# Optimization experiments

Measured on AMD Instinct MI355X. Metric: run time of the kernel, lower is better.

Reference implementation:

```python
import jax, jax.numpy as jnp
import numpy as np

T, HID, H, KV, D = 2048, 2048, 16, 8, 128
EPS = 1e-6
THETA = 10000.0


def setup_inputs() -> dict:
    key = jax.random.key(0)
    ks = jax.random.split(key, 6)
    positions = jnp.arange(T, dtype=jnp.int64 if jax.config.jax_enable_x64 else jnp.int32)
    hidden_states = jax.random.normal(ks[0], (T, HID), dtype=jnp.float32)
    scale = 0.02
    Wq = jax.random.normal(ks[1], (HID, H * 2 * D), dtype=jnp.float32) * scale
    Wk = jax.random.normal(ks[2], (HID, KV * D), dtype=jnp.float32) * scale
    Wv = jax.random.normal(ks[3], (HID, KV * D), dtype=jnp.float32) * scale
    Wo = jax.random.normal(ks[4], (H * D, HID), dtype=jnp.float32) * scale
    q_norm_w = jnp.zeros((D,), dtype=jnp.float32)  # torch init: zeros, applied as (1+w)
    k_norm_w = jnp.zeros((D,), dtype=jnp.float32)
    return {"positions": positions, "hidden_states": hidden_states, "Wq": Wq,
            "Wk": Wk, "Wv": Wv, "Wo": Wo, "q_norm_w": q_norm_w, "k_norm_w": k_norm_w}


def _rms_norm(x, w):
    # fp32 RMSNorm with (1 + weight) scaling, per last dim
    xf = x.astype(jnp.float32)
    inv = jax.lax.rsqrt(jnp.mean(xf * xf, axis=-1, keepdims=True) + EPS)
    return (xf * inv * (1.0 + w.astype(jnp.float32))).astype(x.dtype)


def _rope(x, positions):
    # neox-style rotary over full head_dim; x: (T, heads, D)
    half = D // 2
    inv_freq = 1.0 / (THETA ** (jnp.arange(0, half, dtype=jnp.float32) / half))
    freqs = positions.astype(jnp.float32)[:, None] * inv_freq  # (T, half)
    cos = jnp.cos(freqs)[:, None, :]  # (T,1,half)
    sin = jnp.sin(freqs)[:, None, :]
    x1, x2 = x[..., :half], x[..., half:]
    return jnp.concatenate([x1 * cos - x2 * sin, x2 * cos + x1 * sin], axis=-1)


def reference(positions, hidden_states, Wq, Wk, Wv, Wo, q_norm_w, k_norm_w):
    scaling = D ** -0.5
    qg = (hidden_states @ Wq).reshape(T, H, 2 * D)
    q, gate = qg[..., :D], qg[..., D:]              # (T,H,D) each
    k = (hidden_states @ Wk).reshape(T, KV, D)
    v = (hidden_states @ Wv).reshape(T, KV, D)
    q = _rms_norm(q, q_norm_w)
    k = _rms_norm(k, k_norm_w)
    q = _rope(q, positions)
    k = _rope(k, positions)
    # GQA: repeat kv heads
    rep = H // KV
    k = jnp.repeat(k, rep, axis=1)                   # (T,H,D)
    v = jnp.repeat(v, rep, axis=1)
    scores = jnp.einsum('thd,shd->hts', q, k) * scaling  # (H,T,T)
    causal = positions[:, None] >= positions[None, :]     # (T,T)
    scores = jnp.where(causal[None], scores, jnp.finfo(scores.dtype).min)
    probs = jax.nn.softmax(scores, axis=-1)
    o = jnp.einsum('hts,shd->thd', probs, v).reshape(T, H * D)
    o = o * jax.nn.sigmoid(gate.reshape(T, H * D))
    return o @ Wo
```

## Files before the change

### kernel.cpp

```cpp
#include <hip/hip_runtime.h>
#include <stdint.h>
#include <math.h>

#define T_SEQ 2048
#define HID   2048
#define NH    16
#define NKV   8
#define DH    128

typedef __bf16 bf16x8 __attribute__((ext_vector_type(8)));
typedef float  f32x4  __attribute__((ext_vector_type(4)));

__device__ __forceinline__ ushort f2bf(float f) {
  uint32_t u = __float_as_uint(f);
  u += 0x7FFF + ((u >> 16) & 1);
  return (ushort)(u >> 16);
}
__device__ __forceinline__ ushort f2bf_rz(float f) {
  return (ushort)(__float_as_uint(f) >> 16);
}
__device__ __forceinline__ float bf2f(ushort u) {
  return __uint_as_float(((uint32_t)u) << 16);
}
__device__ __forceinline__ void gld16(const void* g, void* l) {
  __builtin_amdgcn_global_load_lds(
      (const __attribute__((address_space(1))) uint32_t*)g,
      (__attribute__((address_space(3))) uint32_t*)l, 16, 0, 0);
}

__global__ __launch_bounds__(256) void prep_kernel(
    const float* __restrict__ hs, const float* __restrict__ Wq,
    const float* __restrict__ Wk, const float* __restrict__ Wv,
    const float* __restrict__ Wo, ushort* __restrict__ hs16,
    ushort* __restrict__ Wqt, ushort* __restrict__ Wkt,
    ushort* __restrict__ Wvt, ushort* __restrict__ Wot) {
  __shared__ float tile[32][33];
  int bid = blockIdx.x;
  if (bid < 4096) {
    int i = (bid * 256 + threadIdx.x) * 4;
    float4 v = *(const float4*)(hs + i);
    ushort4 o = {f2bf(v.x), f2bf(v.y), f2bf(v.z), f2bf(v.w)};
    *(ushort4*)(hs16 + i) = o;
    return;
  }
  bid -= 4096;
  const float* src; ushort* dst; int N, bi, bj;
  if (bid < 8192)       { src = Wq; dst = Wqt; N = 4096; bj = bid & 127; bi = bid >> 7; }
  else if (bid < 10240) { bid -= 8192;  src = Wk; dst = Wkt; N = 1024; bj = bid & 31; bi = bid >> 5; }
  else if (bid < 12288) { bid -= 10240; src = Wv; dst = Wvt; N = 1024; bj = bid & 31; bi = bid >> 5; }
  else                  { bid -= 12288; src = Wo; dst = Wot; N = 2048; bj = bid & 63; bi = bid >> 6; }
  int row = threadIdx.x >> 3, c4 = (threadIdx.x & 7) * 4;
  float4 v = *(const float4*)(src + (size_t)(bi * 32 + row) * N + bj * 32 + c4);
  tile[row][c4 + 0] = v.x; tile[row][c4 + 1] = v.y;
  tile[row][c4 + 2] = v.z; tile[row][c4 + 3] = v.w;
  __syncthreads();
  ushort4 o = {f2bf(tile[c4 + 0][row]), f2bf(tile[c4 + 1][row]),
               f2bf(tile[c4 + 2][row]), f2bf(tile[c4 + 3][row])};
  *(ushort4*)(dst + (size_t)(bj * 32 + row) * HID + bi * 32 + c4) = o;
}

template <int MI>
__device__ __forceinline__ void gemm_loop(
    const ushort* __restrict__ A, const ushort* __restrict__ Bt,
    int K, int m0, int n0, ushort* As, ushort* Bs, f32x4 (*acc)[4]) {
  const int tid = threadIdx.x, lane = tid & 63, w = tid >> 6;
  const int quad = lane >> 4, l15 = lane & 15;
  const int wm = (w >> 1) * (MI * 16), wn = (w & 1) * 64;
  const int srow = tid >> 2, sch = tid & 3;
  for (int k0 = 0; k0 < K; k0 += 32) {
    __syncthreads();
#pragma unroll
    for (int p = 0; p < MI / 2; ++p) {
      int row = p * 64 + srow;
      int gch = sch ^ ((row >> 1) & 3);
      gld16(A + (size_t)(m0 + row) * K + k0 + gch * 8,
            As + (p * 256 + w * 64) * 8);
    }
#pragma unroll
    for (int p = 0; p < 2; ++p) {
      int row = p * 64 + srow;
      int gch = sch ^ ((row >> 1) & 3);
      gld16(Bt + (size_t)(n0 + row) * K + k0 + gch * 8,
            Bs + (p * 256 + w * 64) * 8);
    }
    __syncthreads();
    bf16x8 af[MI], bfr[4];
#pragma unroll
    for (int mi = 0; mi < MI; ++mi) {
      int row = wm + mi * 16 + l15;
      int pch = quad ^ ((row >> 1) & 3);
      af[mi] = *(const bf16x8*)(As + row * 32 + pch * 8);
    }
#pragma unroll
    for (int ni = 0; ni < 4; ++ni) {
      int row = wn + ni * 16 + l15;
      int pch = quad ^ ((row >> 1) & 3);
      bfr[ni] = *(const bf16x8*)(Bs + row * 32 + pch * 8);
    }
#pragma unroll
    for (int mi = 0; mi < MI; ++mi)
#pragma unroll
      for (int ni = 0; ni < 4; ++ni)
        acc[mi][ni] = __builtin_amdgcn_mfma_f32_16x16x32_bf16(
            af[mi], bfr[ni], acc[mi][ni], 0, 0, 0);
  }
}

__device__ __forceinline__ void bf16_store(f32x4 (*acc)[4],
                                           ushort* __restrict__ Cb, int Ncols,
                                           int m0, int n0) {
  const int lane = threadIdx.x & 63, w = threadIdx.x >> 6;
  const int quad = lane >> 4, l15 = lane & 15;
  const int wm = (w >> 1) * 64, wn = (w & 1) * 64;
#pragma unroll
  for (int mi = 0; mi < 4; ++mi)
#pragma unroll
    for (int ni = 0; ni < 4; ++ni)
#pragma unroll
      for (int r = 0; r < 4; ++r) {
        int row = m0 + wm + mi * 16 + quad * 4 + r;
        int col = n0 + wn + ni * 16 + l15;
        Cb[(size_t)row * Ncols + col] = f2bf(acc[mi][ni][r]);
      }
}

__device__ __forceinline__ void norm_rope_epilogue(
    f32x4 (*acc)[4], const float* __restrict__ wgt,
    const int* __restrict__ positions, int m0, ushort* __restrict__ outp,
    int ostride, char* smem) {
  ushort* tile = (ushort*)smem;
  float* ssum = (float*)(smem + 34816);
  const int tid = threadIdx.x, lane = tid & 63, w = tid >> 6;
  const int quad = lane >> 4, l15 = lane & 15;
  const int wm = (w >> 1) * 64, wn = (w & 1) * 64;
  float sp[4][4];
#pragma unroll
  for (int mi = 0; mi < 4; ++mi)
#pragma unroll
    for (int r = 0; r < 4; ++r) {
      float s = 0.f;
#pragma unroll
      for (int ni = 0; ni < 4; ++ni) { float v = acc[mi][ni][r]; s += v * v; }
#pragma unroll
      for (int off = 1; off <= 8; off <<= 1) s += __shfl_xor(s, off, 64);
      sp[mi][r] = s;
    }
  if (l15 == 0) {
#pragma unroll
    for (int mi = 0; mi < 4; ++mi)
#pragma unroll
      for (int r = 0; r < 4; ++r)
        ssum[(w & 1) * 128 + wm + mi * 16 + quad * 4 + r] = sp[mi][r];
  }
  __syncthreads();
  float wv[4];
#pragma unroll
  for (int ni = 0; ni < 4; ++ni) wv[ni] = 1.f + wgt[wn + ni * 16 + l15];
#pragma unroll
  for (int mi = 0; mi < 4; ++mi)
#pragma unroll
    for (int r = 0; r < 4; ++r) {
      int row = wm + mi * 16 + quad * 4 + r;
      float inv = rsqrtf((ssum[row] + ssum[128 + row]) * (1.f / 128.f) + 1e-6f);
#pragma unroll
      for (int ni = 0; ni < 4; ++ni)
        tile[row * 136 + wn + ni * 16 + l15] =
            f2bf(acc[mi][ni][r] * inv * wv[ni]);
    }
  __syncthreads();
  const int row = tid >> 1, d0 = (tid & 1) * 32;
  const float pos = (float)positions[m0 + row];
  __align__(16) ushort lo[32], hi[32];
#pragma unroll
  for (int j = 0; j < 32; ++j) {
    int d = d0 + j;
    float rev = pos * exp2f((float)d * -0.20762050593045233f) *
                0.15915494309189535f;
    float fr = rev - floorf(rev);
    float s = __builtin_amdgcn_sinf(fr);
    float c = __builtin_amdgcn_cosf(fr);
    float x1 = bf2f(tile[row * 136 + d]);
    float x2 = bf2f(tile[row * 136 + d + 64]);
    lo[j] = f2bf(x1 * c - x2 * s);
    hi[j] = f2bf(x2 * c + x1 * s);
  }
  ushort* op = outp + (size_t)(m0 + row) * ostride + d0;
#pragma unroll
  for (int j = 0; j < 4; ++j) {
    *((uint4*)op + j)        = ((const uint4*)lo)[j];
    *((uint4*)(op + 64) + j) = ((const uint4*)hi)[j];
  }
}

__global__ __launch_bounds__(256) void gemm_qkv(
    const ushort* __restrict__ hs16, const ushort* __restrict__ Wqt,
    const ushort* __restrict__ Wkt, const ushort* __restrict__ Wvt,
    const int* __restrict__ positions, const float* __restrict__ qnw,
    const float* __restrict__ knw, ushort* __restrict__ q16,
    ushort* __restrict__ gate16, ushort* __restrict__ k16,
    ushort* __restrict__ v16t) {
  __shared__ __align__(16) char smem[35840 + 1024];
  ushort* As = (ushort*)smem;
  ushort* Bs = As + 4096;
  f32x4 acc[4][4];
#pragma unroll
  for (int i = 0; i < 4; ++i)
#pragma unroll
    for (int j = 0; j < 4; ++j) acc[i][j] = (f32x4){0.f, 0.f, 0.f, 0.f};
  const int b = blockIdx.x;
  if (b < 512) {
    int mt = b >> 5, nt = b & 31, m0 = mt * 128, h = nt >> 1;
    gemm_loop<4>(hs16, Wqt, HID, m0, nt * 128, As, Bs, acc);
    if ((nt & 1) == 0)
      norm_rope_epilogue(acc, qnw, positions, m0, q16 + h * DH, NH * DH, smem);
    else
      bf16_store(acc, gate16, NH * DH, m0, h * DH);
  } else if (b < 640) {
    int f = b - 512, mt = f >> 3, nt = f & 7, m0 = mt * 128;
    gemm_loop<4>(hs16, Wkt, HID, m0, nt * 128, As, Bs, acc);
    norm_rope_epilogue(acc, knw, positions, m0, k16 + nt * DH, NKV * DH, smem);
  } else {
    int f = b - 640, mt = f >> 4, nt = f & 15;
    gemm_loop<4>(Wvt, hs16, HID, mt * 128, nt * 128, As, Bs, acc);
    bf16_store(acc, v16t, T_SEQ, mt * 128, nt * 128);
  }
}

__global__ __launch_bounds__(256) void gemm_out(
    const ushort* __restrict__ ob16, const ushort* __restrict__ Wot,
    float* __restrict__ out) {
  __shared__ ushort As[64 * 32];
  __shared__ ushort Bs[128 * 32];
  f32x4 acc[2][4];
#pragma unroll
  for (int i = 0; i < 2; ++i)
#pragma unroll
    for (int j = 0; j < 4; ++j) acc[i][j] = (f32x4){0.f, 0.f, 0.f, 0.f};
  const int b = blockIdx.x;
  const int m0 = (b >> 4) * 64, n0 = (b & 15) * 128;
  gemm_loop<2>(ob16, Wot, HID, m0, n0, As, Bs, acc);
  const int lane = threadIdx.x & 63, w = threadIdx.x >> 6;
  const int quad = lane >> 4, l15 = lane & 15;
  const int wm = (w >> 1) * 32, wn = (w & 1) * 64;
#pragma unroll
  for (int mi = 0; mi < 2; ++mi)
#pragma unroll
    for (int ni = 0; ni < 4; ++ni)
#pragma unroll
      for (int r = 0; r < 4; ++r) {
        int row = m0 + wm + mi * 16 + quad * 4 + r;
        int col = n0 + wn + ni * 16 + l15;
        out[(size_t)row * HID + col] = acc[mi][ni][r];
      }
}

__global__ __launch_bounds__(256) void attn_mfma(
    const ushort* __restrict__ q16, const ushort* __restrict__ k16,
    const ushort* __restrict__ v16t, const float* __restrict__ qnw,
    const float* __restrict__ knw, ushort* __restrict__ Op0,
    ushort* __restrict__ Op1, float* __restrict__ lpart) {
  const int pb = blockIdx.x, h = blockIdx.y, s = blockIdx.z, kvh = h >> 1;
  const int tid = threadIdx.x, lane = tid & 63, w = tid >> 6;
  const int quad = lane >> 4, l15 = lane & 15;

  __shared__ ushort Ks[2][64 * 128];
  __shared__ ushort Vs[2][144 * 64];
  __shared__ ushort Ps[4][16][72];

#pragma unroll
  for (int buf = 0; buf < 2; ++buf)
    for (int i = tid; i < 16 * 64; i += 256) {
      int row = 128 + (i >> 6), col = i & 63;
      Vs[buf][row * 64 + col] = (row == 128) ? (ushort)0x3F80 : (ushort)0;
    }

  __shared__ float s8[8];
  __shared__ float bshare;
  {
    float mq = 0.f, mk = 0.f;
    if (tid < 128) { mq = fabsf(1.f + qnw[tid]); mk = fabsf(1.f + knw[tid]); }
#pragma unroll
    for (int off = 32; off >= 1; off >>= 1) {
      mq = fmaxf(mq, __shfl_xor(mq, off, 64));
      mk = fmaxf(mk, __shfl_xor(mk, off, 64));
    }
    if (lane == 0) { s8[w * 2] = mq; s8[w * 2 + 1] = mk; }
    __syncthreads();
    if (tid == 0) {
      float MQ = fmaxf(s8[0], s8[2]), MK = fmaxf(s8[1], s8[3]);
      bshare = 16.3217f * MQ * MK * 1.02f + 0.1f;
    }
    __syncthreads();
  }
  const float B = bshare;
  const float CSC = 0.08838834764831845f * 1.44269504088896f;

#pragma unroll 1
  for (int sel = 0; sel < 2; ++sel) {
    const int qt = sel ? (31 - pb) : pb;
    const int q0 = qt * 64, nk = qt + 1;
    const int ntl = (nk > s) ? ((nk - s + 1) >> 1) : 0;

    bf16x8 qf[4];
    const ushort* qbase = q16 + ((size_t)(q0 + w * 16 + l15) * NH + h) * DH;
#pragma unroll
    for (int ks = 0; ks < 4; ++ks)
      qf[ks] = *(const bf16x8*)(qbase + ks * 32 + quad * 8);

    f32x4 oacc[9];
#pragma unroll
    for (int i = 0; i < 9; ++i) oacc[i] = (f32x4){0.f, 0.f, 0.f, 0.f};

    __syncthreads();
    if (ntl > 0) {
      const int kt0 = s * 64;
#pragma unroll
      for (int p = 0; p < 4; ++p) {
        int row = p * 16 + (tid >> 4), ch = tid & 15;
        int gch = ch ^ (row & 15);
        gld16(k16 + ((size_t)(kt0 + row) * NKV + kvh) * DH + gch * 8,
              (ushort*)Ks[0] + (p * 256 + w * 64) * 8);
      }
#pragma unroll
      for (int p = 0; p < 4; ++p) {
        int row = p * 32 + (tid >> 3), ch = tid & 7;
        int gch = ch ^ (row & 7);
        gld16(v16t + (size_t)(kvh * DH + row) * T_SEQ + kt0 + gch * 8,
              (ushort*)Vs[0] + (p * 256 + w * 64) * 8);
      }
    }

#pragma unroll 1
    for (int it = 0; it < ntl; ++it) {
      const int kt = s + 2 * it;
      const int cur = it & 1;
      __syncthreads();
      if (it + 1 < ntl) {
        const int nt0 = (kt + 2) * 64;
#pragma unroll
        for (int p = 0; p < 4; ++p) {
          int row = p * 16 + (tid >> 4), ch = tid & 15;
          int gch = ch ^ (row & 15);
          gld16(k16 + ((size_t)(nt0 + row) * NKV + kvh) * DH + gch * 8,
                (ushort*)Ks[1 - cur] + (p * 256 + w * 64) * 8);
        }
#pragma unroll
        for (int p = 0; p < 4; ++p) {
          int row = p * 32 + (tid >> 3), ch = tid & 7;
          int gch = ch ^ (row & 7);
          gld16(v16t + (size_t)(kvh * DH + row) * T_SEQ + nt0 + gch * 8,
                (ushort*)Vs[1 - cur] + (p * 256 + w * 64) * 8);
        }
      }

      f32x4 sacc[4];
#pragma unroll
      for (int ni = 0; ni < 4; ++ni) sacc[ni] = (f32x4){0.f, 0.f, 0.f, 0.f};
      const ushort* KsC = Ks[cur];
#pragma unroll
      for (int ks = 0; ks < 4; ++ks)
#pragma unroll
        for (int ni = 0; ni < 4; ++ni) {
          int row = ni * 16 + l15;
          int pch = (ks * 4 + quad) ^ (row & 15);
          bf16x8 kf = *(const bf16x8*)(KsC + row * 128 + pch * 8);
          sacc[ni] = __builtin_amdgcn_mfma_f32_16x16x32_bf16(
              qf[ks], kf, sacc[ni], 0, 0, 0);
        }

      const bool diag = (kt == qt);
      const int kt0 = kt * 64;
#pragma unroll
      for (int ni = 0; ni < 4; ++ni) {
        int key = kt0 + ni * 16 + l15;
#pragma unroll
        for (int r = 0; r < 4; ++r) {
          float arg = fmaf(sacc[ni][r], CSC, -B);
          float pv;
          if (diag) {
            int q = q0 + w * 16 + quad * 4 + r;
            pv = (key <= q) ? exp2f(arg) : 0.f;
          } else {
            pv = exp2f(arg);
          }
          Ps[w][quad * 4 + r][ni * 16 + l15] = f2bf_rz(pv);
        }
      }

      const ushort* VsC = Vs[cur];
#pragma unroll
      for (int ks2 = 0; ks2 < 2; ++ks2) {
        bf16x8 pf = *(const bf16x8*)(&Ps[w][l15][ks2 * 32 + quad * 8]);
#pragma unroll
        for (int ni = 0; ni < 9; ++ni) {
          int row = ni * 16 + l15;
          int pch = (ks2 * 4 + quad) ^ (row & 7);
          bf16x8 vf = *(const bf16x8*)(VsC + row * 64 + pch * 8);
          oacc[ni] = __builtin_amdgcn_mfma_f32_16x16x32_bf16(
              pf, vf, oacc[ni], 0, 0, 0);
        }
      }
    }

    ushort* Op = s ? Op1 : Op0;
#pragma unroll
    for (int ni = 0; ni < 8; ++ni) {
      int d = ni * 16 + l15;
#pragma unroll
      for (int r = 0; r < 4; ++r) {
        int q = q0 + w * 16 + quad * 4 + r;
        Op[((size_t)h * T_SEQ + q) * DH + d] = f2bf(oacc[ni][r]);
      }
    }
    if (l15 == 0) {
#pragma unroll
      for (int r = 0; r < 4; ++r) {
        int q = q0 + w * 16 + quad * 4 + r;
        lpart[(size_t)s * (NH * T_SEQ) + h * T_SEQ + q] = oacc[8][r];
      }
    }
  }
}

__global__ __launch_bounds__(256) void combine_kernel(
    const ushort* __restrict__ Op0, const ushort* __restrict__ Op1,
    const float* __restrict__ lpart, const ushort* __restrict__ gate16,
    ushort* __restrict__ ob16) {
  const int t = blockIdx.x, tid = threadIdx.x;
  const int h = tid >> 4, d0 = (tid & 15) * 8;
  const float l = lpart[h * T_SEQ + t] + lpart[NH * T_SEQ + h * T_SEQ + t];
  const float inv = 1.0f / l;
  const size_t po = ((size_t)h * T_SEQ + t) * DH + d0;
  ushort4 a0 = *(const ushort4*)(Op0 + po);
  ushort4 a1 = *(const ushort4*)(Op0 + po + 4);
  ushort4 b0 = *(const ushort4*)(Op1 + po);
  ushort4 b1 = *(const ushort4*)(Op1 + po + 4);
  const ushort* gp = gate16 + (size_t)t * (NH * DH) + h * DH + d0;
  ushort4 g0 = *(const ushort4*)(gp);
  ushort4 g1 = *(const ushort4*)(gp + 4);
  float oa[8] = {bf2f(a0.x), bf2f(a0.y), bf2f(a0.z), bf2f(a0.w),
                 bf2f(a1.x), bf2f(a1.y), bf2f(a1.z), bf2f(a1.w)};
  float ob[8] = {bf2f(b0.x), bf2f(b0.y), bf2f(b0.z), bf2f(b0.w),
                 bf2f(b1.x), bf2f(b1.y), bf2f(b1.z), bf2f(b1.w)};
  float gg[8] = {bf2f(g0.x), bf2f(g0.y), bf2f(g0.z), bf2f(g0.w),
                 bf2f(g1.x), bf2f(g1.y), bf2f(g1.z), bf2f(g1.w)};
  ushort r[8];
#pragma unroll
  for (int i = 0; i < 8; ++i) {
    float o = (oa[i] + ob[i]) * inv;
    o = o / (1.0f + exp2f(-gg[i] * 1.44269504088896f));
    r[i] = f2bf(o);
  }
  ushort* op = ob16 + (size_t)t * (NH * DH) + h * DH + d0;
  *(ushort4*)(op)     = (ushort4){r[0], r[1], r[2], r[3]};
  *(ushort4*)(op + 4) = (ushort4){r[4], r[5], r[6], r[7]};
}

extern "C" void kernel_launch(void* const* d_in, const int* in_sizes, int n_in,
                              void* d_out, int out_size, void* d_ws, size_t ws_size,
                              hipStream_t stream) {
  const int*   positions = (const int*)d_in[0];
  const float* hs  = (const float*)d_in[1];
  const float* Wq  = (const float*)d_in[2];
  const float* Wk  = (const float*)d_in[3];
  const float* Wv  = (const float*)d_in[4];
  const float* Wo  = (const float*)d_in[5];
  const float* qnw = (const float*)d_in[6];
  const float* knw = (const float*)d_in[7];
  float* out = (float*)d_out;

  const size_t MB = 1 << 20;
  uint8_t* ws = (uint8_t*)d_ws;
  ushort* hs16  = (ushort*)(ws + 0);
  ushort* Op0   = (ushort*)(ws + 0);
  ushort* Wqt   = (ushort*)(ws + 8 * MB);
  ushort* Op1   = (ushort*)(ws + 8 * MB);
  ushort* ob16  = (ushort*)(ws + 16 * MB);
  ushort* Wkt   = (ushort*)(ws + 24 * MB);
  float*  lpart = (float*)(ws + 24 * MB);
  ushort* Wvt   = (ushort*)(ws + 28 * MB);
  ushort* gate16= (ushort*)(ws + 32 * MB);
  ushort* q16   = (ushort*)(ws + 40 * MB);
  ushort* k16   = (ushort*)(ws + 48 * MB);
  ushort* v16t  = (ushort*)(ws + 52 * MB);
  ushort* Wot   = (ushort*)(ws + 56 * MB);

  prep_kernel<<<20480, 256, 0, stream>>>(hs, Wq, Wk, Wv, Wo,
                                         hs16, Wqt, Wkt, Wvt, Wot);
  gemm_qkv<<<768, 256, 0, stream>>>(hs16, Wqt, Wkt, Wvt, positions, qnw, knw,
                                    q16, gate16, k16, v16t);
  attn_mfma<<<dim3(16, NH, 2), 256, 0, stream>>>(q16, k16, v16t, qnw, knw,
                                                 Op0, Op1, lpart);
  combine_kernel<<<T_SEQ, 256, 0, stream>>>(Op0, Op1, lpart, gate16, ob16);
  gemm_out<<<512, 256, 0, stream>>>(ob16, Wot, out);
}
```

Before: 297.5 us.

## Split attention KV across three slices, move q norm/rope into attention, add norm_k kernel

Several changes land together. The weight transpose in prep uses 64x64 tiles with wider stores. The QKV GEMM now writes raw bf16 outputs, and a separate norm_k kernel applies RMSNorm and rope to K. Q norm and rope are folded into the attention kernel's Q load. The KV split goes from 2 to 3 slices with single buffering, which drops the K/V prefetch double-buffer, and combine now sums three partials. The goal is more attention parallelism and a lighter GEMM epilogue, at the cost of an extra launch, lost load/compute overlap, and more partial-output traffic.

```diff
diff --git a/kernel.cpp b/kernel.cpp
--- a/kernel.cpp
+++ b/kernel.cpp
@@ -34,7 +34,6 @@
     const float* __restrict__ Wo, ushort* __restrict__ hs16,
     ushort* __restrict__ Wqt, ushort* __restrict__ Wkt,
     ushort* __restrict__ Wvt, ushort* __restrict__ Wot) {
-  __shared__ float tile[32][33];
   int bid = blockIdx.x;
   if (bid < 4096) {
     int i = (bid * 256 + threadIdx.x) * 4;
@@ -45,18 +44,28 @@
   }
   bid -= 4096;
   const float* src; ushort* dst; int N, bi, bj;
-  if (bid < 8192)       { src = Wq; dst = Wqt; N = 4096; bj = bid & 127; bi = bid >> 7; }
-  else if (bid < 10240) { bid -= 8192;  src = Wk; dst = Wkt; N = 1024; bj = bid & 31; bi = bid >> 5; }
-  else if (bid < 12288) { bid -= 10240; src = Wv; dst = Wvt; N = 1024; bj = bid & 31; bi = bid >> 5; }
-  else                  { bid -= 12288; src = Wo; dst = Wot; N = 2048; bj = bid & 63; bi = bid >> 6; }
-  int row = threadIdx.x >> 3, c4 = (threadIdx.x & 7) * 4;
-  float4 v = *(const float4*)(src + (size_t)(bi * 32 + row) * N + bj * 32 + c4);
-  tile[row][c4 + 0] = v.x; tile[row][c4 + 1] = v.y;
-  tile[row][c4 + 2] = v.z; tile[row][c4 + 3] = v.w;
+  if (bid < 2048)      { src = Wq; dst = Wqt; N = 4096; bj = bid & 63; bi = bid >> 6; }
+  else if (bid < 2560) { bid -= 2048; src = Wk; dst = Wkt; N = 1024; bj = bid & 15; bi = bid >> 4; }
+  else if (bid < 3072) { bid -= 2560; src = Wv; dst = Wvt; N = 1024; bj = bid & 15; bi = bid >> 4; }
+  else                 { bid -= 3072; src = Wo; dst = Wot; N = 2048; bj = bid & 31; bi = bid >> 5; }
+  __shared__ float tile[64][65];
+  const int r = threadIdx.x >> 2, cg = (threadIdx.x & 3) * 16;
+  const float* sp = src + (size_t)(bi * 64 + r) * N + bj * 64 + cg;
+#pragma unroll
+  for (int p = 0; p < 4; ++p) {
+    float4 v = *(const float4*)(sp + p * 4);
+    tile[r][cg + p * 4 + 0] = v.x; tile[r][cg + p * 4 + 1] = v.y;
+    tile[r][cg + p * 4 + 2] = v.z; tile[r][cg + p * 4 + 3] = v.w;
+  }
   __syncthreads();
-  ushort4 o = {f2bf(tile[c4 + 0][row]), f2bf(tile[c4 + 1][row]),
-               f2bf(tile[c4 + 2][row]), f2bf(tile[c4 + 3][row])};
-  *(ushort4*)(dst + (size_t)(bj * 32 + row) * HID + bi * 32 + c4) = o;
+  ushort* dp = dst + (size_t)(bj * 64 + r) * HID + bi * 64 + cg;
+#pragma unroll
+  for (int p = 0; p < 2; ++p) {
+    union { uint4 v; ushort u[8]; } o;
+#pragma unroll
+    for (int j = 0; j < 8; ++j) o.u[j] = f2bf(tile[cg + p * 8 + j][r]);
+    *(uint4*)(dp + p * 8) = o.v;
+  }
 }
 
 template <int MI>
@@ -124,84 +133,13 @@
       }
 }
 
-__device__ __forceinline__ void norm_rope_epilogue(
-    f32x4 (*acc)[4], const float* __restrict__ wgt,
-    const int* __restrict__ positions, int m0, ushort* __restrict__ outp,
-    int ostride, char* smem) {
-  ushort* tile = (ushort*)smem;
-  float* ssum = (float*)(smem + 34816);
-  const int tid = threadIdx.x, lane = tid & 63, w = tid >> 6;
-  const int quad = lane >> 4, l15 = lane & 15;
-  const int wm = (w >> 1) * 64, wn = (w & 1) * 64;
-  float sp[4][4];
-#pragma unroll
-  for (int mi = 0; mi < 4; ++mi)
-#pragma unroll
-    for (int r = 0; r < 4; ++r) {
-      float s = 0.f;
-#pragma unroll
-      for (int ni = 0; ni < 4; ++ni) { float v = acc[mi][ni][r]; s += v * v; }
-#pragma unroll
-      for (int off = 1; off <= 8; off <<= 1) s += __shfl_xor(s, off, 64);
-      sp[mi][r] = s;
-    }
-  if (l15 == 0) {
-#pragma unroll
-    for (int mi = 0; mi < 4; ++mi)
-#pragma unroll
-      for (int r = 0; r < 4; ++r)
-        ssum[(w & 1) * 128 + wm + mi * 16 + quad * 4 + r] = sp[mi][r];
-  }
-  __syncthreads();
-  float wv[4];
-#pragma unroll
-  for (int ni = 0; ni < 4; ++ni) wv[ni] = 1.f + wgt[wn + ni * 16 + l15];
-#pragma unroll
-  for (int mi = 0; mi < 4; ++mi)
-#pragma unroll
-    for (int r = 0; r < 4; ++r) {
-      int row = wm + mi * 16 + quad * 4 + r;
-      float inv = rsqrtf((ssum[row] + ssum[128 + row]) * (1.f / 128.f) + 1e-6f);
-#pragma unroll
-      for (int ni = 0; ni < 4; ++ni)
-        tile[row * 136 + wn + ni * 16 + l15] =
-            f2bf(acc[mi][ni][r] * inv * wv[ni]);
-    }
-  __syncthreads();
-  const int row = tid >> 1, d0 = (tid & 1) * 32;
-  const float pos = (float)positions[m0 + row];
-  __align__(16) ushort lo[32], hi[32];
-#pragma unroll
-  for (int j = 0; j < 32; ++j) {
-    int d = d0 + j;
-    float rev = pos * exp2f((float)d * -0.20762050593045233f) *
-                0.15915494309189535f;
-    float fr = rev - floorf(rev);
-    float s = __builtin_amdgcn_sinf(fr);
-    float c = __builtin_amdgcn_cosf(fr);
-    float x1 = bf2f(tile[row * 136 + d]);
-    float x2 = bf2f(tile[row * 136 + d + 64]);
-    lo[j] = f2bf(x1 * c - x2 * s);
-    hi[j] = f2bf(x2 * c + x1 * s);
-  }
-  ushort* op = outp + (size_t)(m0 + row) * ostride + d0;
-#pragma unroll
-  for (int j = 0; j < 4; ++j) {
-    *((uint4*)op + j)        = ((const uint4*)lo)[j];
-    *((uint4*)(op + 64) + j) = ((const uint4*)hi)[j];
-  }
-}
-
 __global__ __launch_bounds__(256) void gemm_qkv(
     const ushort* __restrict__ hs16, const ushort* __restrict__ Wqt,
     const ushort* __restrict__ Wkt, const ushort* __restrict__ Wvt,
-    const int* __restrict__ positions, const float* __restrict__ qnw,
-    const float* __restrict__ knw, ushort* __restrict__ q16,
-    ushort* __restrict__ gate16, ushort* __restrict__ k16,
+    ushort* __restrict__ qg16, ushort* __restrict__ kb16,
     ushort* __restrict__ v16t) {
-  __shared__ __align__(16) char smem[35840 + 1024];
-  ushort* As = (ushort*)smem;
-  ushort* Bs = As + 4096;
+  __shared__ ushort As[128 * 32];
+  __shared__ ushort Bs[128 * 32];
   f32x4 acc[4][4];
 #pragma unroll
   for (int i = 0; i < 4; ++i)
@@ -209,20 +147,17 @@
     for (int j = 0; j < 4; ++j) acc[i][j] = (f32x4){0.f, 0.f, 0.f, 0.f};
   const int b = blockIdx.x;
   if (b < 512) {
-    int mt = b >> 5, nt = b & 31, m0 = mt * 128, h = nt >> 1;
-    gemm_loop<4>(hs16, Wqt, HID, m0, nt * 128, As, Bs, acc);
-    if ((nt & 1) == 0)
-      norm_rope_epilogue(acc, qnw, positions, m0, q16 + h * DH, NH * DH, smem);
-    else
-      bf16_store(acc, gate16, NH * DH, m0, h * DH);
+    int m0 = (b >> 5) * 128, n0 = (b & 31) * 128;
+    gemm_loop<4>(hs16, Wqt, HID, m0, n0, As, Bs, acc);
+    bf16_store(acc, qg16, 4096, m0, n0);
   } else if (b < 640) {
-    int f = b - 512, mt = f >> 3, nt = f & 7, m0 = mt * 128;
-    gemm_loop<4>(hs16, Wkt, HID, m0, nt * 128, As, Bs, acc);
-    norm_rope_epilogue(acc, knw, positions, m0, k16 + nt * DH, NKV * DH, smem);
+    int f = b - 512, m0 = (f >> 3) * 128, n0 = (f & 7) * 128;
+    gemm_loop<4>(hs16, Wkt, HID, m0, n0, As, Bs, acc);
+    bf16_store(acc, kb16, 1024, m0, n0);
   } else {
-    int f = b - 640, mt = f >> 4, nt = f & 15;
-    gemm_loop<4>(Wvt, hs16, HID, mt * 128, nt * 128, As, Bs, acc);
-    bf16_store(acc, v16t, T_SEQ, mt * 128, nt * 128);
+    int f = b - 640, m0 = (f >> 4) * 128, n0 = (f & 15) * 128;
+    gemm_loop<4>(Wvt, hs16, HID, m0, n0, As, Bs, acc);
+    bf16_store(acc, v16t, T_SEQ, m0, n0);
   }
 }
 
@@ -254,25 +189,55 @@
       }
 }
 
+__global__ __launch_bounds__(128) void norm_k(
+    const ushort* __restrict__ kb16, const int* __restrict__ positions,
+    const float* __restrict__ kw, ushort* __restrict__ k16) {
+  const int t = blockIdx.x, kv = blockIdx.y, d = threadIdx.x;
+  const ushort* x = kb16 + ((size_t)t * NKV + kv) * DH;
+  ushort* out = k16 + ((size_t)t * NKV + kv) * DH;
+  float v = bf2f(x[d]);
+  float ss = v * v;
+#pragma unroll
+  for (int off = 32; off >= 1; off >>= 1) ss += __shfl_xor(ss, off, 64);
+  __shared__ float red[2];
+  if ((d & 63) == 0) red[d >> 6] = ss;
+  __syncthreads();
+  float mean = (red[0] + red[1]) * (1.0f / 128.0f);
+  float xn = v * rsqrtf(mean + 1e-6f) * (1.0f + kw[d]);
+  __shared__ float sh[128];
+  sh[d] = xn;
+  __syncthreads();
+  if (d < 64) {
+    float pos = (float)positions[t];
+    float rev = pos * exp2f((float)d * -0.20762050593045233f) *
+                0.15915494309189535f;
+    float fr = rev - floorf(rev);
+    float s = __builtin_amdgcn_sinf(fr);
+    float c = __builtin_amdgcn_cosf(fr);
+    float x1 = sh[d], x2 = sh[d + 64];
+    out[d]      = f2bf(x1 * c - x2 * s);
+    out[d + 64] = f2bf(x2 * c + x1 * s);
+  }
+}
+
 __global__ __launch_bounds__(256) void attn_mfma(
-    const ushort* __restrict__ q16, const ushort* __restrict__ k16,
-    const ushort* __restrict__ v16t, const float* __restrict__ qnw,
-    const float* __restrict__ knw, ushort* __restrict__ Op0,
-    ushort* __restrict__ Op1, float* __restrict__ lpart) {
+    const ushort* __restrict__ qg16, const ushort* __restrict__ k16,
+    const ushort* __restrict__ v16t, const int* __restrict__ positions,
+    const float* __restrict__ qnw, const float* __restrict__ knw,
+    ushort* __restrict__ Op0, ushort* __restrict__ Op1,
+    ushort* __restrict__ Op2, float* __restrict__ lpart) {
   const int pb = blockIdx.x, h = blockIdx.y, s = blockIdx.z, kvh = h >> 1;
   const int tid = threadIdx.x, lane = tid & 63, w = tid >> 6;
   const int quad = lane >> 4, l15 = lane & 15;
 
-  __shared__ ushort Ks[2][64 * 128];
-  __shared__ ushort Vs[2][144 * 64];
+  __shared__ ushort Ks[64 * 128];
+  __shared__ ushort Vs[144 * 64];
   __shared__ ushort Ps[4][16][72];
 
-#pragma unroll
-  for (int buf = 0; buf < 2; ++buf)
-    for (int i = tid; i < 16 * 64; i += 256) {
-      int row = 128 + (i >> 6), col = i & 63;
-      Vs[buf][row * 64 + col] = (row == 128) ? (ushort)0x3F80 : (ushort)0;
-    }
+  for (int i = tid; i < 16 * 64; i += 256) {
+    int row = 128 + (i >> 6), col = i & 63;
+    Vs[row * 64 + col] = (row == 128) ? (ushort)0x3F80 : (ushort)0;
+  }
 
   __shared__ float s8[8];
   __shared__ float bshare;
@@ -295,81 +260,95 @@
   const float B = bshare;
   const float CSC = 0.08838834764831845f * 1.44269504088896f;
 
+  float wq[4][8];
+#pragma unroll
+  for (int ks = 0; ks < 4; ++ks)
+#pragma unroll
+    for (int j = 0; j < 8; ++j) wq[ks][j] = 1.f + qnw[ks * 32 + quad * 8 + j];
+
 #pragma unroll 1
   for (int sel = 0; sel < 2; ++sel) {
     const int qt = sel ? (31 - pb) : pb;
-    const int q0 = qt * 64, nk = qt + 1;
-    const int ntl = (nk > s) ? ((nk - s + 1) >> 1) : 0;
-
-    bf16x8 qf[4];
-    const ushort* qbase = q16 + ((size_t)(q0 + w * 16 + l15) * NH + h) * DH;
+    const int q0 = qt * 64;
+    const int ntl = (qt >= s) ? ((qt - s) / 3 + 1) : 0;
+
+    float qv[4][8];
+    const ushort* qb = qg16 + ((size_t)(q0 + w * 16 + l15) * NH + h) * (2 * DH);
+#pragma unroll
+    for (int ks = 0; ks < 4; ++ks) {
+      ushort4 u0 = *(const ushort4*)(qb + ks * 32 + quad * 8);
+      ushort4 u1 = *(const ushort4*)(qb + ks * 32 + quad * 8 + 4);
+      qv[ks][0] = bf2f(u0.x); qv[ks][1] = bf2f(u0.y);
+      qv[ks][2] = bf2f(u0.z); qv[ks][3] = bf2f(u0.w);
+      qv[ks][4] = bf2f(u1.x); qv[ks][5] = bf2f(u1.y);
+      qv[ks][6] = bf2f(u1.z); qv[ks][7] = bf2f(u1.w);
+    }
+    float ss = 0.f;
 #pragma unroll
     for (int ks = 0; ks < 4; ++ks)
-      qf[ks] = *(const bf16x8*)(qbase + ks * 32 + quad * 8);
+#pragma unroll
+      for (int j = 0; j < 8; ++j) ss += qv[ks][j] * qv[ks][j];
+    ss += __shfl_xor(ss, 16, 64);
+    ss += __shfl_xor(ss, 32, 64);
+    const float inv = rsqrtf(ss * (1.f / 128.f) + 1e-6f);
+    const float pos = (float)positions[q0 + w * 16 + l15];
+    union { bf16x8 v; ushort u[8]; } qfu[4];
+#pragma unroll
+    for (int ks = 0; ks < 2; ++ks)
+#pragma unroll
+      for (int j = 0; j < 8; ++j) {
+        int d = ks * 32 + quad * 8 + j;
+        float rev = pos * exp2f((float)d * -0.20762050593045233f) *
+                    0.15915494309189535f;
+        float fr = rev - floorf(rev);
+        float sn = __builtin_amdgcn_sinf(fr);
+        float cs = __builtin_amdgcn_cosf(fr);
+        float x1 = qv[ks][j] * inv * wq[ks][j];
+        float x2 = qv[ks + 2][j] * inv * wq[ks + 2][j];
+        qfu[ks].u[j]     = f2bf(x1 * cs - x2 * sn);
+        qfu[ks + 2].u[j] = f2bf(x2 * cs + x1 * sn);
+      }
 
     f32x4 oacc[9];
 #pragma unroll
     for (int i = 0; i < 9; ++i) oacc[i] = (f32x4){0.f, 0.f, 0.f, 0.f};
 
-    __syncthreads();
-    if (ntl > 0) {
-      const int kt0 = s * 64;
+#pragma unroll 1
+    for (int it = 0; it < ntl; ++it) {
+      const int kt = s + 3 * it;
+      const int kt0 = kt * 64;
+      __syncthreads();
 #pragma unroll
       for (int p = 0; p < 4; ++p) {
         int row = p * 16 + (tid >> 4), ch = tid & 15;
         int gch = ch ^ (row & 15);
         gld16(k16 + ((size_t)(kt0 + row) * NKV + kvh) * DH + gch * 8,
-              (ushort*)Ks[0] + (p * 256 + w * 64) * 8);
+              Ks + (p * 256 + w * 64) * 8);
       }
 #pragma unroll
       for (int p = 0; p < 4; ++p) {
         int row = p * 32 + (tid >> 3), ch = tid & 7;
         int gch = ch ^ (row & 7);
         gld16(v16t + (size_t)(kvh * DH + row) * T_SEQ + kt0 + gch * 8,
-              (ushort*)Vs[0] + (p * 256 + w * 64) * 8);
-      }
-    }
-
-#pragma unroll 1
-    for (int it = 0; it < ntl; ++it) {
-      const int kt = s + 2 * it;
-      const int cur = it & 1;
+              Vs + (p * 256 + w * 64) * 8);
+      }
       __syncthreads();
-      if (it + 1 < ntl) {
-        const int nt0 = (kt + 2) * 64;
-#pragma unroll
-        for (int p = 0; p < 4; ++p) {
-          int row = p * 16 + (tid >> 4), ch = tid & 15;
-          int gch = ch ^ (row & 15);
-          gld16(k16 + ((size_t)(nt0 + row) * NKV + kvh) * DH + gch * 8,
-                (ushort*)Ks[1 - cur] + (p * 256 + w * 64) * 8);
-        }
-#pragma unroll
-        for (int p = 0; p < 4; ++p) {
-          int row = p * 32 + (tid >> 3), ch = tid & 7;
-          int gch = ch ^ (row & 7);
-          gld16(v16t + (size_t)(kvh * DH + row) * T_SEQ + nt0 + gch * 8,
-                (ushort*)Vs[1 - cur] + (p * 256 + w * 64) * 8);
-        }
-      }
 
       f32x4 sacc[4];
 #pragma unroll
       for (int ni = 0; ni < 4; ++ni) sacc[ni] = (f32x4){0.f, 0.f, 0.f, 0.f};
-      const ushort* KsC = Ks[cur];
 #pragma unroll
       for (int ks = 0; ks < 4; ++ks)
 #pragma unroll
         for (int ni = 0; ni < 4; ++ni) {
           int row = ni * 16 + l15;
           int pch = (ks * 4 + quad) ^ (row & 15);
-          bf16x8 kf = *(const bf16x8*)(KsC + row * 128 + pch * 8);
+          bf16x8 kf = *(const bf16x8*)(Ks + row * 128 + pch * 8);
           sacc[ni] = __builtin_amdgcn_mfma_f32_16x16x32_bf16(
-              qf[ks], kf, sacc[ni], 0, 0, 0);
+              qfu[ks].v, kf, sacc[ni], 0, 0, 0);
         }
 
       const bool diag = (kt == qt);
-      const int kt0 = kt * 64;
 #pragma unroll
       for (int ni = 0; ni < 4; ++ni) {
         int key = kt0 + ni * 16 + l15;
@@ -387,7 +366,6 @@
         }
       }
 
-      const ushort* VsC = Vs[cur];
 #pragma unroll
       for (int ks2 = 0; ks2 < 2; ++ks2) {
         bf16x8 pf = *(const bf16x8*)(&Ps[w][l15][ks2 * 32 + quad * 8]);
@@ -395,14 +373,14 @@
         for (int ni = 0; ni < 9; ++ni) {
           int row = ni * 16 + l15;
           int pch = (ks2 * 4 + quad) ^ (row & 7);
-          bf16x8 vf = *(const bf16x8*)(VsC + row * 64 + pch * 8);
+          bf16x8 vf = *(const bf16x8*)(Vs + row * 64 + pch * 8);
           oacc[ni] = __builtin_amdgcn_mfma_f32_16x16x32_bf16(
               pf, vf, oacc[ni], 0, 0, 0);
         }
       }
     }
 
-    ushort* Op = s ? Op1 : Op0;
+    ushort* Op = (s == 0) ? Op0 : (s == 1) ? Op1 : Op2;
 #pragma unroll
     for (int ni = 0; ni < 8; ++ni) {
       int d = ni * 16 + l15;
@@ -424,30 +402,36 @@
 
 __global__ __launch_bounds__(256) void combine_kernel(
     const ushort* __restrict__ Op0, const ushort* __restrict__ Op1,
-    const float* __restrict__ lpart, const ushort* __restrict__ gate16,
-    ushort* __restrict__ ob16) {
+    const ushort* __restrict__ Op2, const float* __restrict__ lpart,
+    const ushort* __restrict__ qg16, ushort* __restrict__ ob16) {
   const int t = blockIdx.x, tid = threadIdx.x;
   const int h = tid >> 4, d0 = (tid & 15) * 8;
-  const float l = lpart[h * T_SEQ + t] + lpart[NH * T_SEQ + h * T_SEQ + t];
+  const int NT = NH * T_SEQ;
+  const float l = lpart[h * T_SEQ + t] + lpart[NT + h * T_SEQ + t] +
+                  lpart[2 * NT + h * T_SEQ + t];
   const float inv = 1.0f / l;
   const size_t po = ((size_t)h * T_SEQ + t) * DH + d0;
   ushort4 a0 = *(const ushort4*)(Op0 + po);
   ushort4 a1 = *(const ushort4*)(Op0 + po + 4);
   ushort4 b0 = *(const ushort4*)(Op1 + po);
   ushort4 b1 = *(const ushort4*)(Op1 + po + 4);
-  const ushort* gp = gate16 + (size_t)t * (NH * DH) + h * DH + d0;
+  ushort4 c0 = *(const ushort4*)(Op2 + po);
+  ushort4 c1 = *(const ushort4*)(Op2 + po + 4);
+  const ushort* gp = qg16 + ((size_t)t * NH + h) * (2 * DH) + DH + d0;
   ushort4 g0 = *(const ushort4*)(gp);
   ushort4 g1 = *(const ushort4*)(gp + 4);
   float oa[8] = {bf2f(a0.x), bf2f(a0.y), bf2f(a0.z), bf2f(a0.w),
                  bf2f(a1.x), bf2f(a1.y), bf2f(a1.z), bf2f(a1.w)};
   float ob[8] = {bf2f(b0.x), bf2f(b0.y), bf2f(b0.z), bf2f(b0.w),
                  bf2f(b1.x), bf2f(b1.y), bf2f(b1.z), bf2f(b1.w)};
+  float oc[8] = {bf2f(c0.x), bf2f(c0.y), bf2f(c0.z), bf2f(c0.w),
+                 bf2f(c1.x), bf2f(c1.y), bf2f(c1.z), bf2f(c1.w)};
   float gg[8] = {bf2f(g0.x), bf2f(g0.y), bf2f(g0.z), bf2f(g0.w),
                  bf2f(g1.x), bf2f(g1.y), bf2f(g1.z), bf2f(g1.w)};
   ushort r[8];
 #pragma unroll
   for (int i = 0; i < 8; ++i) {
-    float o = (oa[i] + ob[i]) * inv;
+    float o = (oa[i] + ob[i] + oc[i]) * inv;
     o = o / (1.0f + exp2f(-gg[i] * 1.44269504088896f));
     r[i] = f2bf(o);
   }
@@ -471,26 +455,27 @@
 
   const size_t MB = 1 << 20;
   uint8_t* ws = (uint8_t*)d_ws;
-  ushort* hs16  = (ushort*)(ws + 0);
-  ushort* Op0   = (ushort*)(ws + 0);
-  ushort* Wqt   = (ushort*)(ws + 8 * MB);
-  ushort* Op1   = (ushort*)(ws + 8 * MB);
-  ushort* ob16  = (ushort*)(ws + 16 * MB);
-  ushort* Wkt   = (ushort*)(ws + 24 * MB);
-  float*  lpart = (float*)(ws + 24 * MB);
-  ushort* Wvt   = (ushort*)(ws + 28 * MB);
-  ushort* gate16= (ushort*)(ws + 32 * MB);
-  ushort* q16   = (ushort*)(ws + 40 * MB);
-  ushort* k16   = (ushort*)(ws + 48 * MB);
-  ushort* v16t  = (ushort*)(ws + 52 * MB);
-  ushort* Wot   = (ushort*)(ws + 56 * MB);
-
-  prep_kernel<<<20480, 256, 0, stream>>>(hs, Wq, Wk, Wv, Wo,
-                                         hs16, Wqt, Wkt, Wvt, Wot);
-  gemm_qkv<<<768, 256, 0, stream>>>(hs16, Wqt, Wkt, Wvt, positions, qnw, knw,
-                                    q16, gate16, k16, v16t);
-  attn_mfma<<<dim3(16, NH, 2), 256, 0, stream>>>(q16, k16, v16t, qnw, knw,
-                                                 Op0, Op1, lpart);
-  combine_kernel<<<T_SEQ, 256, 0, stream>>>(Op0, Op1, lpart, gate16, ob16);
+  ushort* qg16 = (ushort*)(ws + 0);
+  ushort* hs16 = (ushort*)(ws + 16 * MB);
+  ushort* Op0  = (ushort*)(ws + 16 * MB);
+  ushort* Wqt  = (ushort*)(ws + 24 * MB);
+  ushort* Op1  = (ushort*)(ws + 24 * MB);
+  ushort* Op2  = (ushort*)(ws + 32 * MB);
+  ushort* kb16 = (ushort*)(ws + 40 * MB);
+  float*  lpart= (float*)(ws + 40 * MB);
+  ushort* Wkt  = (ushort*)(ws + 44 * MB);
+  ushort* k16  = (ushort*)(ws + 44 * MB);
+  ushort* Wvt  = (ushort*)(ws + 48 * MB);
+  ushort* ob16 = (ushort*)(ws + 48 * MB);
+  ushort* v16t = (ushort*)(ws + 52 * MB);
+  ushort* Wot  = (ushort*)(ws + 56 * MB);
+
+  prep_kernel<<<8192, 256, 0, stream>>>(hs, Wq, Wk, Wv, Wo,
+                                        hs16, Wqt, Wkt, Wvt, Wot);
+  gemm_qkv<<<768, 256, 0, stream>>>(hs16, Wqt, Wkt, Wvt, qg16, kb16, v16t);
+  norm_k<<<dim3(T_SEQ, NKV), 128, 0, stream>>>(kb16, positions, knw, k16);
+  attn_mfma<<<dim3(16, NH, 3), 256, 0, stream>>>(qg16, k16, v16t, positions,
+                                                 qnw, knw, Op0, Op1, Op2, lpart);
+  combine_kernel<<<T_SEQ, 256, 0, stream>>>(Op0, Op1, Op2, lpart, qg16, ob16);
   gemm_out<<<512, 256, 0, stream>>>(ob16, Wot, out);
 }
```

New measurement: 289.5 us. -2.7%, faster.
